# Kernel optimization log

Measured on AMD Instinct MI355X. Metric: run time of the kernel, lower is better.

## Reference

```python
import jax, jax.numpy as jnp
import numpy as np

D_MODEL = 1024
NHEAD = 16
HEAD_DIM = D_MODEL // NHEAD


def setup_inputs() -> dict:
    key = jax.random.key(0)
    ks = jax.random.split(key, 11)
    B, S = 4, 2048
    s = 1.0 / np.sqrt(D_MODEL)
    return {
        "q": jax.random.normal(ks[0], (B, S, D_MODEL), jnp.float32),
        "k": jax.random.normal(ks[1], (B, S, D_MODEL), jnp.float32),
        "v": jax.random.normal(ks[2], (B, S, D_MODEL), jnp.float32),
        "Wq": jax.random.normal(ks[3], (D_MODEL, D_MODEL), jnp.float32) * s,
        "bq": jnp.zeros((D_MODEL,), jnp.float32),
        "Wk": jax.random.normal(ks[4], (D_MODEL, D_MODEL), jnp.float32) * s,
        "bk": jnp.zeros((D_MODEL,), jnp.float32),
        "Wv": jax.random.normal(ks[5], (D_MODEL, D_MODEL), jnp.float32) * s,
        "bv": jnp.zeros((D_MODEL,), jnp.float32),
        "Wo": jax.random.normal(ks[6], (D_MODEL, D_MODEL), jnp.float32) * s,
        "bo": jnp.zeros((D_MODEL,), jnp.float32),
    }


def reference(q, k, v, Wq, bq, Wk, bk, Wv, bv, Wo, bo):
    B, S, _ = q.shape
    H, Dh = NHEAD, HEAD_DIM

    def proj(x, W, b):  # nn.Linear: x @ W.T + b, then split heads -> [B,H,S,Dh]
        y = x @ W.T + b
        return y.reshape(B, S, H, Dh).transpose(0, 2, 1, 3)

    qh = proj(q, Wq, bq)
    kh = proj(k, Wk, bk)
    vh = proj(v, Wv, bv)

    scores = jnp.einsum("bhsd,bhtd->bhst", qh, kh) / jnp.sqrt(jnp.float32(Dh))
    attn = jax.nn.softmax(scores, axis=-1)
    out = jnp.einsum("bhst,bhtd->bhsd", attn, vh)  # [B,H,S,Dh]
    out = out.transpose(0, 2, 1, 3).reshape(B, S, H * Dh)
    return out @ Wo.T + bo
```

## Files before the change

kernel.cpp:

```cpp
#include <hip/hip_runtime.h>


typedef short bf16x8 __attribute__((ext_vector_type(8)));
typedef short bf16x4 __attribute__((ext_vector_type(4)));
typedef float f32x4 __attribute__((ext_vector_type(4)));

__device__ __forceinline__ short f2bf(float x) {
    union { float f; unsigned int u; } un; un.f = x;
    unsigned int u = un.u;
    return (short)(unsigned short)((u + 0x7fffu + ((u >> 16) & 1u)) >> 16);
}

__device__ __forceinline__ void gll16(const void* g, void* l) {
    __builtin_amdgcn_global_load_lds(
        (const __attribute__((address_space(1))) void*)g,
        (__attribute__((address_space(3))) void*)l, 16, 0, 0);
}

struct CvtArgs { const float* s[4]; unsigned short* d[4]; int n4; };
__global__ __launch_bounds__(256) void cvt_bf16(CvtArgs ca) {
    const float* s = ca.s[blockIdx.y];
    unsigned short* d = ca.d[blockIdx.y];
    int i = blockIdx.x * blockDim.x + threadIdx.x;
    int stride = gridDim.x * blockDim.x;
    const float4* s4 = reinterpret_cast<const float4*>(s);
    bf16x4* d4 = reinterpret_cast<bf16x4*>(d);
    for (; i < ca.n4; i += stride) {
        float4 x = s4[i];
        bf16x4 y;
        y[0] = f2bf(x.x); y[1] = f2bf(x.y); y[2] = f2bf(x.z); y[3] = f2bf(x.w);
        d4[i] = y;
    }
}

__device__ __forceinline__ void gemm_core(const unsigned short* __restrict__ A,
                                          const unsigned short* __restrict__ W,
                                          const float* __restrict__ bias,
                                          float scale, void* __restrict__ out,
                                          int mode) {
    __shared__ unsigned short As[128 * 64];
    __shared__ unsigned short Bs[128 * 64];
    const int tid = threadIdx.x;
    const int m0 = blockIdx.y * 128, n0 = blockIdx.x * 128;
    const int wave = tid >> 6, lane = tid & 63;
    const int wm = (wave >> 1) * 64, wn = (wave & 1) * 64;
    const int l15 = lane & 15, quad = lane >> 4;
    const int srow = tid >> 3;
    const int scol = ((tid & 7) ^ (srow & 7)) * 8;
    const int cb = (l15 & 7);

    f32x4 acc[4][4] = {};

    for (int k0 = 0; k0 < 1024; k0 += 64) {
        __syncthreads();
#pragma unroll
        for (int ro = 0; ro < 4; ++ro) {
            gll16(&A[(size_t)(m0 + ro * 32 + srow) * 1024 + k0 + scol], &As[ro * 2048 + tid * 8]);
            gll16(&W[(size_t)(n0 + ro * 32 + srow) * 1024 + k0 + scol], &Bs[ro * 2048 + tid * 8]);
        }
        __syncthreads();
#pragma unroll
        for (int kk = 0; kk < 2; ++kk) {
            const int co = ((4 * kk + quad) ^ cb) * 8;
            bf16x8 a[4], b[4];
#pragma unroll
            for (int i = 0; i < 4; ++i)
                a[i] = *reinterpret_cast<bf16x8*>(&As[(wm + i * 16 + l15) * 64 + co]);
#pragma unroll
            for (int j = 0; j < 4; ++j)
                b[j] = *reinterpret_cast<bf16x8*>(&Bs[(wn + j * 16 + l15) * 64 + co]);
#pragma unroll
            for (int i = 0; i < 4; ++i)
#pragma unroll
                for (int j = 0; j < 4; ++j)
                    acc[i][j] = __builtin_amdgcn_mfma_f32_16x16x32_bf16(a[i], b[j], acc[i][j], 0, 0, 0);
        }
    }

#pragma unroll
    for (int i = 0; i < 4; ++i) {
#pragma unroll
        for (int j = 0; j < 4; ++j) {
#pragma unroll
            for (int r = 0; r < 4; ++r) {
                int m = m0 + wm + i * 16 + quad * 4 + r;
                int n = n0 + wn + j * 16 + l15;
                float val = (acc[i][j][r] + bias[n]) * scale;
                if (mode == 0) {
                    reinterpret_cast<float*>(out)[(size_t)m * 1024 + n] = val;
                } else {
                    int b_ = m >> 11, s = m & 2047, h = n >> 6, d = n & 63;
                    size_t off = (mode == 1)
                                     ? ((size_t)((b_ * 16 + h) * 2048 + s) * 64 + d)
                                     : ((size_t)((b_ * 16 + h) * 64 + d) * 2048 + s);
                    reinterpret_cast<unsigned short*>(out)[off] = (unsigned short)f2bf(val);
                }
            }
        }
    }
}

struct QkvArgs {
    const unsigned short* A[3];
    const unsigned short* W[3];
    const float* bias[3];
    float scale[3];
    unsigned short* out[3];
    int mode[3];
};
__global__ __launch_bounds__(256) void gemm_qkv(QkvArgs ga) {
    int z = blockIdx.z;
    gemm_core(ga.A[z], ga.W[z], ga.bias[z], ga.scale[z], ga.out[z], ga.mode[z]);
}

__global__ __launch_bounds__(256) void gemm_wo(const unsigned short* __restrict__ A,
                                               const unsigned short* __restrict__ W,
                                               const float* __restrict__ bias,
                                               float* __restrict__ out) {
    gemm_core(A, W, bias, 1.0f, out, 0);
}

__global__ __launch_bounds__(256, 3) void flash_attn(const unsigned short* __restrict__ Qh,
                                                     const unsigned short* __restrict__ Kh,
                                                     const unsigned short* __restrict__ Vt,
                                                     unsigned short* __restrict__ Oa) {
    constexpr int LD = 72;
    __shared__ unsigned short Ks[2][64 * 64];
    __shared__ unsigned short Vs[2][64 * 64];
    __shared__ unsigned short Ps[4 * 32 * LD];
    const int tid = threadIdx.x;
    const int bh = blockIdx.y;
    const int q0 = blockIdx.x * 128;
    const unsigned short* Qb = Qh + (size_t)bh * 2048 * 64;
    const unsigned short* Kb = Kh + (size_t)bh * 2048 * 64;
    const unsigned short* Vb = Vt + (size_t)bh * 64 * 2048;
    const int wave = tid >> 6, lane = tid & 63;
    const int l15 = lane & 15, quad = lane >> 4;
    const int wq = wave * 32;
    const int srow = tid >> 3;
    const int scol = ((tid & 7) ^ (srow & 7)) * 8;
    const int cb = (l15 & 7);
    unsigned short* Pw = &Ps[wave * 32 * LD];

    bf16x8 qreg[2][2];
#pragma unroll
    for (int i = 0; i < 2; ++i)
#pragma unroll
        for (int kk = 0; kk < 2; ++kk)
            qreg[i][kk] = *reinterpret_cast<const bf16x8*>(
                &Qb[(size_t)(q0 + wq + i * 16 + l15) * 64 + kk * 32 + quad * 8]);

    bf16x8 ones;
#pragma unroll
    for (int j = 0; j < 8; ++j) ones[j] = (short)0x3F80;

    f32x4 o[2][4] = {};
    f32x4 lacc[2] = {};

#pragma unroll
    for (int ro = 0; ro < 2; ++ro) {
        gll16(&Kb[(size_t)(ro * 32 + srow) * 64 + scol], &Ks[0][ro * 2048 + tid * 8]);
        gll16(&Vb[(size_t)(ro * 32 + srow) * 2048 + scol], &Vs[0][ro * 2048 + tid * 8]);
    }
    __syncthreads();

    for (int it = 0; it < 32; ++it) {
        const int buf = it & 1;
        if (it < 31) {
            int kvn = (it + 1) * 64;
#pragma unroll
            for (int ro = 0; ro < 2; ++ro) {
                gll16(&Kb[(size_t)(kvn + ro * 32 + srow) * 64 + scol], &Ks[buf ^ 1][ro * 2048 + tid * 8]);
                gll16(&Vb[(size_t)(ro * 32 + srow) * 2048 + kvn + scol], &Vs[buf ^ 1][ro * 2048 + tid * 8]);
            }
        }

        f32x4 sacc[2][4] = {};
#pragma unroll
        for (int kk = 0; kk < 2; ++kk) {
            const int co = ((4 * kk + quad) ^ cb) * 8;
            bf16x8 ak[4];
#pragma unroll
            for (int j = 0; j < 4; ++j)
                ak[j] = *reinterpret_cast<bf16x8*>(&Ks[buf][(j * 16 + l15) * 64 + co]);
#pragma unroll
            for (int i = 0; i < 2; ++i)
#pragma unroll
                for (int j = 0; j < 4; ++j)
                    sacc[i][j] = __builtin_amdgcn_mfma_f32_16x16x32_bf16(ak[j], qreg[i][kk], sacc[i][j], 0, 0, 0);
        }

#pragma unroll
        for (int i = 0; i < 2; ++i) {
#pragma unroll
            for (int j = 0; j < 4; ++j) {
                float p0 = __builtin_amdgcn_exp2f(sacc[i][j][0]);
                float p1 = __builtin_amdgcn_exp2f(sacc[i][j][1]);
                float p2 = __builtin_amdgcn_exp2f(sacc[i][j][2]);
                float p3 = __builtin_amdgcn_exp2f(sacc[i][j][3]);
                union { float f; unsigned u; } a0{p0}, a1{p1}, a2{p2}, a3{p3};
                unsigned lo = __builtin_amdgcn_perm(a1.u + 0x8000u, a0.u + 0x8000u, 0x07060302u);
                unsigned hi = __builtin_amdgcn_perm(a3.u + 0x8000u, a2.u + 0x8000u, 0x07060302u);
                uint2 pk; pk.x = lo; pk.y = hi;
                *reinterpret_cast<uint2*>(&Pw[(i * 16 + l15) * LD + j * 16 + quad * 4]) = pk;
            }
        }

#pragma unroll
        for (int kk = 0; kk < 2; ++kk) {
            const int co = ((4 * kk + quad) ^ cb) * 8;
            bf16x8 ap[2];
#pragma unroll
            for (int i = 0; i < 2; ++i)
                ap[i] = *reinterpret_cast<bf16x8*>(&Pw[(i * 16 + l15) * LD + kk * 32 + quad * 8]);
#pragma unroll
            for (int i = 0; i < 2; ++i)
                lacc[i] = __builtin_amdgcn_mfma_f32_16x16x32_bf16(ap[i], ones, lacc[i], 0, 0, 0);
#pragma unroll
            for (int n = 0; n < 4; ++n) {
                bf16x8 bv = *reinterpret_cast<bf16x8*>(&Vs[buf][(n * 16 + l15) * 64 + co]);
#pragma unroll
                for (int i = 0; i < 2; ++i)
                    o[i][n] = __builtin_amdgcn_mfma_f32_16x16x32_bf16(ap[i], bv, o[i][n], 0, 0, 0);
            }
        }
        __syncthreads();
    }

    const int b_ = bh >> 4, h = bh & 15;
#pragma unroll
    for (int i = 0; i < 2; ++i) {
        f32x4 rv;
#pragma unroll
        for (int r = 0; r < 4; ++r) rv[r] = 1.0f / lacc[i][r];
#pragma unroll
        for (int n = 0; n < 4; ++n)
#pragma unroll
            for (int r = 0; r < 4; ++r) {
                int s = q0 + wq + i * 16 + quad * 4 + r;
                int d = n * 16 + l15;
                Oa[(size_t)(b_ * 2048 + s) * 1024 + h * 64 + d] =
                    (unsigned short)f2bf(o[i][n][r] * rv[r]);
            }
    }
}

extern "C" void kernel_launch(void* const* d_in, const int* in_sizes, int n_in,
                              void* d_out, int out_size, void* d_ws, size_t ws_size,
                              hipStream_t stream) {
    const float* q  = (const float*)d_in[0];
    const float* k  = (const float*)d_in[1];
    const float* v  = (const float*)d_in[2];
    const float* Wq = (const float*)d_in[3];
    const float* bq = (const float*)d_in[4];
    const float* Wk = (const float*)d_in[5];
    const float* bk = (const float*)d_in[6];
    const float* Wv = (const float*)d_in[7];
    const float* bv = (const float*)d_in[8];
    const float* Wo = (const float*)d_in[9];
    const float* bo = (const float*)d_in[10];

    const size_t E = (size_t)8192 * 1024;
    const size_t WE = (size_t)1024 * 1024;
    unsigned short* r0 = (unsigned short*)d_ws;
    unsigned short* r1 = r0 + E;
    unsigned short* r2 = r1 + E;
    unsigned short* r3 = r2 + E;
    unsigned short* wqb = r3 + E;
    unsigned short* wkb = wqb + WE;
    unsigned short* wvb = wkb + WE;
    unsigned short* wob = wvb + WE;

    CvtArgs ca;
    ca.s[0] = q; ca.d[0] = r0;
    ca.s[1] = k; ca.d[1] = r1;
    ca.s[2] = v; ca.d[2] = r2;
    ca.s[3] = q; ca.d[3] = r0;
    ca.n4 = (int)(E / 4);
    cvt_bf16<<<dim3(1024, 3), 256, 0, stream>>>(ca);

    CvtArgs cw;
    cw.s[0] = Wq; cw.d[0] = wqb;
    cw.s[1] = Wk; cw.d[1] = wkb;
    cw.s[2] = Wv; cw.d[2] = wvb;
    cw.s[3] = Wo; cw.d[3] = wob;
    cw.n4 = (int)(WE / 4);
    cvt_bf16<<<dim3(256, 4), 256, 0, stream>>>(cw);

    const float QSCALE = 0.125f * 1.44269504088896340736f;

    QkvArgs ga;
    ga.A[0] = r0; ga.W[0] = wqb; ga.bias[0] = bq; ga.scale[0] = QSCALE; ga.out[0] = r3; ga.mode[0] = 1;
    ga.A[1] = r1; ga.W[1] = wkb; ga.bias[1] = bk; ga.scale[1] = 1.0f;   ga.out[1] = r0; ga.mode[1] = 1;
    ga.A[2] = r2; ga.W[2] = wvb; ga.bias[2] = bv; ga.scale[2] = 1.0f;   ga.out[2] = r1; ga.mode[2] = 2;
    gemm_qkv<<<dim3(8, 64, 3), 256, 0, stream>>>(ga);

    flash_attn<<<dim3(16, 64), 256, 0, stream>>>(r3, r0, r1, r2);
    gemm_wo<<<dim3(8, 64), 256, 0, stream>>>(r2, wob, bo, (float*)d_out);
}
```

Before: 375.8 us.

## Switch flash attention to 32x32 MFMA with register-resident P via permlane swap

The attention kernel now uses 32x32x16 bf16 MFMA tiles computing S^T (K rows by query columns), so each lane holds one query's scores. The exponentiated probabilities are packed to bf16 and rearranged across lane halves with v_permlane32_swap, which lets them feed the PV MFMA straight from registers instead of going through an LDS staging buffer. The row sum is accumulated with plain adds rather than an extra MFMA against a ones vector. This removes LDS writes and reads for P and the ones-MFMAs, but depends on getting the permlane layout mapping right and uses larger accumulators, which raises register pressure.

```diff
diff --git a/kernel.cpp b/kernel.cpp
--- a/kernel.cpp
+++ b/kernel.cpp
@@ -4,6 +4,8 @@
 typedef short bf16x8 __attribute__((ext_vector_type(8)));
 typedef short bf16x4 __attribute__((ext_vector_type(4)));
 typedef float f32x4 __attribute__((ext_vector_type(4)));
+typedef float f32x16 __attribute__((ext_vector_type(16)));
+typedef unsigned int u32x4 __attribute__((ext_vector_type(4)));
 
 __device__ __forceinline__ short f2bf(float x) {
     union { float f; unsigned int u; } un; un.f = x;
@@ -15,6 +17,10 @@
     __builtin_amdgcn_global_load_lds(
         (const __attribute__((address_space(1))) void*)g,
         (__attribute__((address_space(3))) void*)l, 16, 0, 0);
+}
+
+__device__ __forceinline__ void plswap(unsigned& a, unsigned& b) {
+    asm("v_permlane32_swap_b32 %0, %1" : "+v"(a), "+v"(b));
 }
 
 struct CvtArgs { const float* s[4]; unsigned short* d[4]; int n4; };
@@ -124,10 +130,8 @@
                                                      const unsigned short* __restrict__ Kh,
                                                      const unsigned short* __restrict__ Vt,
                                                      unsigned short* __restrict__ Oa) {
-    constexpr int LD = 72;
     __shared__ unsigned short Ks[2][64 * 64];
     __shared__ unsigned short Vs[2][64 * 64];
-    __shared__ unsigned short Ps[4 * 32 * LD];
     const int tid = threadIdx.x;
     const int bh = blockIdx.y;
     const int q0 = blockIdx.x * 128;
@@ -135,27 +139,25 @@
     const unsigned short* Kb = Kh + (size_t)bh * 2048 * 64;
     const unsigned short* Vb = Vt + (size_t)bh * 64 * 2048;
     const int wave = tid >> 6, lane = tid & 63;
-    const int l15 = lane & 15, quad = lane >> 4;
+    const int l31 = lane & 31, hi = lane >> 5;
     const int wq = wave * 32;
     const int srow = tid >> 3;
     const int scol = ((tid & 7) ^ (srow & 7)) * 8;
-    const int cb = (l15 & 7);
-    unsigned short* Pw = &Ps[wave * 32 * LD];
-
-    bf16x8 qreg[2][2];
-#pragma unroll
-    for (int i = 0; i < 2; ++i)
-#pragma unroll
-        for (int kk = 0; kk < 2; ++kk)
-            qreg[i][kk] = *reinterpret_cast<const bf16x8*>(
-                &Qb[(size_t)(q0 + wq + i * 16 + l15) * 64 + kk * 32 + quad * 8]);
-
-    bf16x8 ones;
-#pragma unroll
-    for (int j = 0; j < 8; ++j) ones[j] = (short)0x3F80;
-
-    f32x4 o[2][4] = {};
-    f32x4 lacc[2] = {};
+
+    int chx[4], rowoff[2];
+#pragma unroll
+    for (int c = 0; c < 4; ++c) chx[c] = ((c * 2 + hi) ^ (l31 & 7)) * 8;
+    rowoff[0] = l31 * 64;
+    rowoff[1] = (32 + l31) * 64;
+
+    bf16x8 qreg[4];
+#pragma unroll
+    for (int c = 0; c < 4; ++c)
+        qreg[c] = *reinterpret_cast<const bf16x8*>(
+            &Qb[(size_t)(q0 + wq + l31) * 64 + c * 16 + hi * 8]);
+
+    f32x16 o[2] = {};
+    float lacc = 0.f;
 
 #pragma unroll
     for (int ro = 0; ro < 2; ++ro) {
@@ -175,73 +177,65 @@
             }
         }
 
-        f32x4 sacc[2][4] = {};
-#pragma unroll
-        for (int kk = 0; kk < 2; ++kk) {
-            const int co = ((4 * kk + quad) ^ cb) * 8;
-            bf16x8 ak[4];
-#pragma unroll
-            for (int j = 0; j < 4; ++j)
-                ak[j] = *reinterpret_cast<bf16x8*>(&Ks[buf][(j * 16 + l15) * 64 + co]);
-#pragma unroll
-            for (int i = 0; i < 2; ++i)
-#pragma unroll
-                for (int j = 0; j < 4; ++j)
-                    sacc[i][j] = __builtin_amdgcn_mfma_f32_16x16x32_bf16(ak[j], qreg[i][kk], sacc[i][j], 0, 0, 0);
-        }
-
-#pragma unroll
-        for (int i = 0; i < 2; ++i) {
-#pragma unroll
-            for (int j = 0; j < 4; ++j) {
-                float p0 = __builtin_amdgcn_exp2f(sacc[i][j][0]);
-                float p1 = __builtin_amdgcn_exp2f(sacc[i][j][1]);
-                float p2 = __builtin_amdgcn_exp2f(sacc[i][j][2]);
-                float p3 = __builtin_amdgcn_exp2f(sacc[i][j][3]);
-                union { float f; unsigned u; } a0{p0}, a1{p1}, a2{p2}, a3{p3};
-                unsigned lo = __builtin_amdgcn_perm(a1.u + 0x8000u, a0.u + 0x8000u, 0x07060302u);
-                unsigned hi = __builtin_amdgcn_perm(a3.u + 0x8000u, a2.u + 0x8000u, 0x07060302u);
-                uint2 pk; pk.x = lo; pk.y = hi;
-                *reinterpret_cast<uint2*>(&Pw[(i * 16 + l15) * LD + j * 16 + quad * 4]) = pk;
-            }
-        }
-
-#pragma unroll
-        for (int kk = 0; kk < 2; ++kk) {
-            const int co = ((4 * kk + quad) ^ cb) * 8;
-            bf16x8 ap[2];
-#pragma unroll
-            for (int i = 0; i < 2; ++i)
-                ap[i] = *reinterpret_cast<bf16x8*>(&Pw[(i * 16 + l15) * LD + kk * 32 + quad * 8]);
-#pragma unroll
-            for (int i = 0; i < 2; ++i)
-                lacc[i] = __builtin_amdgcn_mfma_f32_16x16x32_bf16(ap[i], ones, lacc[i], 0, 0, 0);
-#pragma unroll
-            for (int n = 0; n < 4; ++n) {
-                bf16x8 bv = *reinterpret_cast<bf16x8*>(&Vs[buf][(n * 16 + l15) * 64 + co]);
-#pragma unroll
-                for (int i = 0; i < 2; ++i)
-                    o[i][n] = __builtin_amdgcn_mfma_f32_16x16x32_bf16(ap[i], bv, o[i][n], 0, 0, 0);
+        f32x16 sacc[2] = {};
+#pragma unroll
+        for (int c = 0; c < 4; ++c) {
+            bf16x8 ak0 = *reinterpret_cast<bf16x8*>(&Ks[buf][rowoff[0] + chx[c]]);
+            bf16x8 ak1 = *reinterpret_cast<bf16x8*>(&Ks[buf][rowoff[1] + chx[c]]);
+            sacc[0] = __builtin_amdgcn_mfma_f32_32x32x16_bf16(ak0, qreg[c], sacc[0], 0, 0, 0);
+            sacc[1] = __builtin_amdgcn_mfma_f32_32x32x16_bf16(ak1, qreg[c], sacc[1], 0, 0, 0);
+        }
+
+        bf16x8 pa[4];
+#pragma unroll
+        for (int mt = 0; mt < 2; ++mt) {
+            float e[16];
+#pragma unroll
+            for (int r = 0; r < 16; ++r) e[r] = __builtin_amdgcn_exp2f(sacc[mt][r]);
+            float s01 = (e[0] + e[1]) + (e[2] + e[3]);
+            float s23 = (e[4] + e[5]) + (e[6] + e[7]);
+            float s45 = (e[8] + e[9]) + (e[10] + e[11]);
+            float s67 = (e[12] + e[13]) + (e[14] + e[15]);
+            lacc += (s01 + s23) + (s45 + s67);
+            unsigned w[8];
+#pragma unroll
+            for (int t = 0; t < 8; ++t) {
+                union { float f; unsigned u; } a0{e[2 * t]}, a1{e[2 * t + 1]};
+                w[t] = __builtin_amdgcn_perm(a1.u + 0x8000u, a0.u + 0x8000u, 0x07060302u);
+            }
+            plswap(w[0], w[2]); plswap(w[1], w[3]);
+            plswap(w[4], w[6]); plswap(w[5], w[7]);
+            u32x4 t0; t0[0] = w[0]; t0[1] = w[1]; t0[2] = w[2]; t0[3] = w[3];
+            u32x4 t1; t1[0] = w[4]; t1[1] = w[5]; t1[2] = w[6]; t1[3] = w[7];
+            pa[mt * 2 + 0] = __builtin_bit_cast(bf16x8, t0);
+            pa[mt * 2 + 1] = __builtin_bit_cast(bf16x8, t1);
+        }
+
+#pragma unroll
+        for (int cg = 0; cg < 4; ++cg) {
+#pragma unroll
+            for (int nt = 0; nt < 2; ++nt) {
+                bf16x8 bv = *reinterpret_cast<bf16x8*>(&Vs[buf][rowoff[nt] + chx[cg]]);
+                o[nt] = __builtin_amdgcn_mfma_f32_32x32x16_bf16(pa[cg], bv, o[nt], 0, 0, 0);
             }
         }
         __syncthreads();
     }
 
+    float lfull = lacc + __shfl_xor(lacc, 32, 64);
+    float rinv = 1.0f / lfull;
     const int b_ = bh >> 4, h = bh & 15;
 #pragma unroll
-    for (int i = 0; i < 2; ++i) {
-        f32x4 rv;
-#pragma unroll
-        for (int r = 0; r < 4; ++r) rv[r] = 1.0f / lacc[i][r];
-#pragma unroll
-        for (int n = 0; n < 4; ++n)
-#pragma unroll
-            for (int r = 0; r < 4; ++r) {
-                int s = q0 + wq + i * 16 + quad * 4 + r;
-                int d = n * 16 + l15;
-                Oa[(size_t)(b_ * 2048 + s) * 1024 + h * 64 + d] =
-                    (unsigned short)f2bf(o[i][n][r] * rv[r]);
-            }
+    for (int r = 0; r < 16; ++r) {
+        const int qrow = (r & 3) + 8 * (r >> 2) + 4 * hi;
+        const float rl = __shfl(rinv, qrow, 64);
+        const int s = q0 + wq + qrow;
+#pragma unroll
+        for (int nt = 0; nt < 2; ++nt) {
+            const int d = nt * 32 + l31;
+            Oa[(size_t)(b_ * 2048 + s) * 1024 + h * 64 + d] =
+                (unsigned short)f2bf(o[nt][r] * rl);
+        }
     }
 }
 
```

New measurement: 377.4 us. No clear change (+0.4%).
